# Performance work log

Hardware: AMD Instinct MI355X
Metric: run time of the kernel (lower is better)

## Reference

```python
import jax, jax.numpy as jnp
import numpy as np

DIM, HEADS, WS, SS = 256, 8, 4, 2
B, D, H, W = 2, 16, 56, 56


def _rel_pos_index(ws):
    coords = np.stack(np.meshgrid(np.arange(ws), np.arange(ws), np.arange(ws), indexing='ij'))
    flat = coords.reshape(3, -1)                      # [3, n]
    rel = (flat[:, :, None] - flat[:, None, :]).transpose(1, 2, 0).astype(np.int64)  # [n,n,3]
    rel[..., 0] += ws - 1; rel[..., 1] += ws - 1; rel[..., 2] += ws - 1
    rel[..., 0] *= (2 * ws - 1) ** 2
    rel[..., 1] *= (2 * ws - 1)
    return rel.sum(-1)                                # [n, n]


def _attn_mask(d, h, w, ws, ss):
    # dims are divisible by ws here, so padded dims == dims (matches torch ceil-pad)
    img = np.zeros((d, h, w))
    sl = (slice(0, -ws), slice(-ws, -ss), slice(-ss, None))
    cnt = 0
    for dsl in sl:
        for hsl in sl:
            for wsl in sl:
                img[dsl, hsl, wsl] = cnt
                cnt += 1
    mw = img.reshape(d // ws, ws, h // ws, ws, w // ws, ws)
    mw = mw.transpose(0, 2, 4, 1, 3, 5).reshape(-1, ws ** 3)   # [nW, n]
    diff = mw[:, None, :] - mw[:, :, None]
    return np.where(diff != 0, -100.0, 0.0).astype(np.float32)  # [nW, n, n]


def _window_partition(x, ws):
    b, d, h, w, c = x.shape
    x = x.reshape(b, d // ws, ws, h // ws, ws, w // ws, ws, c)
    return x.transpose(0, 1, 3, 5, 2, 4, 6, 7).reshape(-1, ws ** 3, c)


def _window_reverse(win, ws, b, d, h, w, c):
    x = win.reshape(b, d // ws, h // ws, w // ws, ws, ws, ws, c)
    return x.transpose(0, 1, 4, 2, 5, 3, 6, 7).reshape(b, d, h, w, c)


def _ln(x, g, b, eps=1e-5):
    mu = x.mean(-1, keepdims=True)
    var = ((x - mu) ** 2).mean(-1, keepdims=True)
    return (x - mu) * jax.lax.rsqrt(var + eps) * g + b


def setup_inputs() -> dict:
    key = jax.random.key(0)
    ks = jax.random.split(key, 8)
    s = 0.02
    return {
        'x': jax.random.normal(ks[0], (B, D, H, W, DIM), jnp.float32),
        'norm1_g': jnp.ones((DIM,), jnp.float32),
        'norm1_b': jnp.zeros((DIM,), jnp.float32),
        'qkv_w': jax.random.normal(ks[1], (DIM, 3 * DIM), jnp.float32) * s,
        'qkv_b': jnp.zeros((3 * DIM,), jnp.float32),
        'proj_w': jax.random.normal(ks[2], (DIM, DIM), jnp.float32) * s,
        'proj_b': jnp.zeros((DIM,), jnp.float32),
        'rpb_table': jax.random.normal(ks[3], ((2 * WS - 1) ** 3, HEADS), jnp.float32) * s,
        'norm2_g': jnp.ones((DIM,), jnp.float32),
        'norm2_b': jnp.zeros((DIM,), jnp.float32),
        'fc1_w': jax.random.normal(ks[4], (DIM, 4 * DIM), jnp.float32) * s,
        'fc1_b': jnp.zeros((4 * DIM,), jnp.float32),
        'fc2_w': jax.random.normal(ks[5], (4 * DIM, DIM), jnp.float32) * s,
        'fc2_b': jnp.zeros((DIM,), jnp.float32),
    }


def reference(x, norm1_g, norm1_b, qkv_w, qkv_b, proj_w, proj_b, rpb_table,
              norm2_g, norm2_b, fc1_w, fc1_b, fc2_w, fc2_b):
    b, d, h, w, c = x.shape
    nh, ws, ss = HEADS, WS, SS
    hd = c // nh
    shortcut = x

    xn = _ln(x, norm1_g, norm1_b)
    xs = jnp.roll(xn, shift=(-ss, -ss, -ss), axis=(1, 2, 3))
    xw = _window_partition(xs, ws)            # [B_, n, c]
    B_, n, _ = xw.shape

    qkv = (xw @ qkv_w + qkv_b).reshape(B_, n, 3, nh, hd).transpose(2, 0, 3, 1, 4)
    q, k, v = qkv[0], qkv[1], qkv[2]          # [B_, nh, n, hd]
    attn = jnp.einsum('bhqd,bhkd->bhqk', q * (hd ** -0.5), k)

    rpi = jnp.asarray(_rel_pos_index(ws).reshape(-1))
    bias = rpb_table[rpi].reshape(n, n, nh).transpose(2, 0, 1)  # [nh, n, n]
    attn = attn + bias[None]

    mask = jnp.asarray(_attn_mask(d, h, w, ws, ss))             # [nW, n, n]
    nW = mask.shape[0]
    attn = attn.reshape(B_ // nW, nW, nh, n, n) + mask[None, :, None]
    attn = jax.nn.softmax(attn.reshape(B_, nh, n, n), axis=-1)

    out = jnp.einsum('bhqk,bhkd->bhqd', attn, v).transpose(0, 2, 1, 3).reshape(B_, n, c)
    out = out @ proj_w + proj_b

    xr = _window_reverse(out, ws, b, d, h, w, c)
    xr = jnp.roll(xr, shift=(ss, ss, ss), axis=(1, 2, 3))
    x1 = shortcut + xr

    y = _ln(x1, norm2_g, norm2_b)
    y = jax.nn.gelu(y @ fc1_w + fc1_b, approximate=False) @ fc2_w + fc2_b
    return x1 + y
```

## Files before the change

kernel.cpp:

```cpp
#include <hip/hip_runtime.h>
#include <math.h>


using f32x4  = __attribute__((ext_vector_type(4))) float;
using bf16x8 = __attribute__((ext_vector_type(8))) short;

__device__ __forceinline__ short f2bf(float f) {
  unsigned u = __builtin_bit_cast(unsigned, f);
  u += 0x7fffu + ((u >> 16) & 1u);
  return (short)(u >> 16);
}

#define GLDS16(g, l) __builtin_amdgcn_global_load_lds(                        \
    (__attribute__((address_space(1))) void*)(g),                             \
    (__attribute__((address_space(3))) void*)(l), 16, 0, 0)

__global__ void transpose_all_k(const float* __restrict__ qkv_w,
                                const float* __restrict__ proj_w,
                                const float* __restrict__ fc1_w,
                                const float* __restrict__ fc2_w,
                                short* __restrict__ o_qkv,
                                short* __restrict__ o_proj,
                                short* __restrict__ o_fc1,
                                short* __restrict__ o_fc2) {
  int bid = blockIdx.x;
  const float* in; short* out; int K, N;
  if (bid < 768)       { in = qkv_w;  out = o_qkv;  K = 256;  N = 768; }
  else if (bid < 1024) { in = proj_w; out = o_proj; K = 256;  N = 256;  bid -= 768; }
  else if (bid < 2048) { in = fc1_w;  out = o_fc1;  K = 256;  N = 1024; bid -= 1024; }
  else                 { in = fc2_w;  out = o_fc2;  K = 1024; N = 256;  bid -= 2048; }
  const int idx = bid * 256 + threadIdx.x;
  const int k = idx / N, n = idx % N;
  out[(size_t)n * K + k] = f2bf(in[idx]);
}

__global__ __launch_bounds__(256) void ln1_part_k(
    const float* __restrict__ x, const float* __restrict__ g,
    const float* __restrict__ bta, short* __restrict__ xw) {
  const int wave = threadIdx.x >> 6, lane = threadIdx.x & 63;
  const int row = blockIdx.x * 4 + wave;
  const int win = row >> 6, tok = row & 63;
  const int b = win / 784, wi = win % 784;
  const int wd = wi / 196, wh = (wi / 14) % 14, ww = wi % 14;
  const int tz = tok >> 4, ty = (tok >> 2) & 3, tx = tok & 3;
  const int gd = (wd * 4 + tz + 2) & 15;
  int gh = wh * 4 + ty + 2; if (gh >= 56) gh -= 56;
  int gw = ww * 4 + tx + 2; if (gw >= 56) gw -= 56;
  const size_t src = ((((size_t)b * 16 + gd) * 56 + gh) * 56 + gw) * 256;
  const float4 v = ((const float4*)(x + src))[lane];
  float s = v.x + v.y + v.z + v.w;
#pragma unroll
  for (int m = 1; m < 64; m <<= 1) s += __shfl_xor(s, m);
  const float mean = s * (1.f / 256.f);
  const float dx = v.x - mean, dy = v.y - mean, dz = v.z - mean, dw = v.w - mean;
  float q = dx * dx + dy * dy + dz * dz + dw * dw;
#pragma unroll
  for (int m = 1; m < 64; m <<= 1) q += __shfl_xor(q, m);
  const float rstd = rsqrtf(q * (1.f / 256.f) + 1e-5f);
  const float4 gg = ((const float4*)g)[lane];
  const float4 bb = ((const float4*)bta)[lane];
  short4 o;
  o.x = f2bf(dx * rstd * gg.x + bb.x);
  o.y = f2bf(dy * rstd * gg.y + bb.y);
  o.z = f2bf(dz * rstd * gg.z + bb.z);
  o.w = f2bf(dw * rstd * gg.w + bb.w);
  *(short4*)(xw + (size_t)row * 256 + lane * 4) = o;
}

__global__ __launch_bounds__(256) void ln2_k(
    const float* __restrict__ x1, const float* __restrict__ g,
    const float* __restrict__ bta, short* __restrict__ yn) {
  const int wave = threadIdx.x >> 6, lane = threadIdx.x & 63;
  const int row = blockIdx.x * 4 + wave;
  const float4 v = ((const float4*)(x1 + (size_t)row * 256))[lane];
  float s = v.x + v.y + v.z + v.w;
#pragma unroll
  for (int m = 1; m < 64; m <<= 1) s += __shfl_xor(s, m);
  const float mean = s * (1.f / 256.f);
  const float dx = v.x - mean, dy = v.y - mean, dz = v.z - mean, dw = v.w - mean;
  float q = dx * dx + dy * dy + dz * dz + dw * dw;
#pragma unroll
  for (int m = 1; m < 64; m <<= 1) q += __shfl_xor(q, m);
  const float rstd = rsqrtf(q * (1.f / 256.f) + 1e-5f);
  const float4 gg = ((const float4*)g)[lane];
  const float4 bb = ((const float4*)bta)[lane];
  short4 o;
  o.x = f2bf(dx * rstd * gg.x + bb.x);
  o.y = f2bf(dy * rstd * gg.y + bb.y);
  o.z = f2bf(dz * rstd * gg.z + bb.z);
  o.w = f2bf(dw * rstd * gg.w + bb.w);
  *(short4*)(yn + (size_t)row * 256 + lane * 4) = o;
}

template <int EPI>
__global__ __launch_bounds__(256) void gemm_k(
    const short* __restrict__ A, const short* __restrict__ Bt,
    const float* __restrict__ bias, const float* __restrict__ resid,
    void* __restrict__ OutP, int N, int K) {
  __shared__ short As[128 * 64];
  __shared__ short Bs[128 * 64];
  const int tid = threadIdx.x;
  const int wave = tid >> 6, lane = tid & 63;
  const int quad = lane >> 4, l15 = lane & 15;
  const int m0 = blockIdx.y * 128;
  const int n0 = blockIdx.x * 128;
  const int wm = (wave >> 1) * 64, wn = (wave & 1) * 64;

  f32x4 acc[4][4] = {};

  for (int k0 = 0; k0 < K; k0 += 64) {
    __syncthreads();
#pragma unroll
    for (int i = 0; i < 4; ++i) {
      const int p = wave * 256 + i * 64 + lane;
      const int row = p >> 3;
      const int c = (p & 7) ^ (row & 7);
      GLDS16(A  + (size_t)(m0 + row) * K + (k0 + c * 8),
             As + (size_t)(wave * 256 + i * 64) * 8);
      GLDS16(Bt + (size_t)(n0 + row) * K + (k0 + c * 8),
             Bs + (size_t)(wave * 256 + i * 64) * 8);
    }
    __syncthreads();
#pragma unroll
    for (int ks = 0; ks < 2; ++ks) {
      bf16x8 af[4], bfr[4];
#pragma unroll
      for (int t = 0; t < 4; ++t) {
        const int ra = wm + t * 16 + l15;
        const int ca = (ks * 4 + quad) ^ (ra & 7);
        af[t] = *(const bf16x8*)(As + ra * 64 + ca * 8);
        const int rb = wn + t * 16 + l15;
        const int cb = (ks * 4 + quad) ^ (rb & 7);
        bfr[t] = *(const bf16x8*)(Bs + rb * 64 + cb * 8);
      }
#pragma unroll
      for (int mt = 0; mt < 4; ++mt)
#pragma unroll
        for (int nt = 0; nt < 4; ++nt)
          acc[mt][nt] = __builtin_amdgcn_mfma_f32_16x16x32_bf16(
              af[mt], bfr[nt], acc[mt][nt], 0, 0, 0);
    }
  }

  if constexpr (EPI == 0 || EPI == 1) {
    short* out = (short*)OutP;
#pragma unroll
    for (int nt = 0; nt < 4; ++nt) {
      const int col = n0 + wn + nt * 16 + l15;
      const float bv = bias[col];
#pragma unroll
      for (int mt = 0; mt < 4; ++mt)
#pragma unroll
        for (int reg = 0; reg < 4; ++reg) {
          const int row = m0 + wm + mt * 16 + quad * 4 + reg;
          float v = acc[mt][nt][reg] + bv;
          if constexpr (EPI == 1)
            v = 0.5f * v * (1.f + erff(v * 0.70710678118654752f));
          out[(size_t)row * N + col] = f2bf(v);
        }
    }
  } else if constexpr (EPI == 2) {
    float* out = (float*)OutP;
#pragma unroll
    for (int nt = 0; nt < 4; ++nt) {
      const int col = n0 + wn + nt * 16 + l15;
      const float bv = bias[col];
#pragma unroll
      for (int mt = 0; mt < 4; ++mt)
#pragma unroll
        for (int reg = 0; reg < 4; ++reg) {
          const int row = m0 + wm + mt * 16 + quad * 4 + reg;
          const int win = row >> 6, tok = row & 63;
          const int b = win / 784, wi = win % 784;
          const int wd = wi / 196, wh = (wi / 14) % 14, ww = wi % 14;
          const int tz = tok >> 4, ty = (tok >> 2) & 3, tx = tok & 3;
          const int gd = (wd * 4 + tz + 2) & 15;
          int gh = wh * 4 + ty + 2; if (gh >= 56) gh -= 56;
          int gw = ww * 4 + tx + 2; if (gw >= 56) gw -= 56;
          const size_t dst =
              ((((size_t)b * 16 + gd) * 56 + gh) * 56 + gw) * 256 + col;
          out[dst] = resid[dst] + acc[mt][nt][reg] + bv;
        }
    }
  } else {
    float* out = (float*)OutP;
#pragma unroll
    for (int nt = 0; nt < 4; ++nt) {
      const int col = n0 + wn + nt * 16 + l15;
      const float bv = bias[col];
#pragma unroll
      for (int mt = 0; mt < 4; ++mt)
#pragma unroll
        for (int reg = 0; reg < 4; ++reg) {
          const int row = m0 + wm + mt * 16 + quad * 4 + reg;
          out[(size_t)row * 256 + col] =
              resid[(size_t)row * 256 + col] + acc[mt][nt][reg] + bv;
        }
    }
  }
}

__global__ __launch_bounds__(256) void attn_k(
    const short* __restrict__ qkv, const float* __restrict__ rpb,
    short* __restrict__ aout) {
  __shared__ short Plds[4 * 64 * 80];
  const int tid = threadIdx.x;
  const int wave = tid >> 6, lane = tid & 63;
  const int quad = lane >> 4, l15 = lane & 15;
  const int win = blockIdx.x >> 1;
  const int h = ((blockIdx.x & 1) << 2) + wave;
  const int wi = win % 784;
  const int wd = wi / 196, wh = (wi / 14) % 14, ww = wi % 14;
  const short* base = qkv + (size_t)win * (64 * 768);

  bf16x8 qf[4], kf[4];
#pragma unroll
  for (int t = 0; t < 4; ++t) {
    const short* qp = base + (size_t)(t * 16 + l15) * 768 + h * 32 + quad * 8;
    qf[t] = *(const bf16x8*)qp;
    kf[t] = *(const bf16x8*)(qp + 256);
  }
  f32x4 S[4][4] = {};
#pragma unroll
  for (int mt = 0; mt < 4; ++mt)
#pragma unroll
    for (int nt = 0; nt < 4; ++nt)
      S[mt][nt] = __builtin_amdgcn_mfma_f32_16x16x32_bf16(
          qf[mt], kf[nt], S[mt][nt], 0, 0, 0);

  const bool bd = (wd == 3), bh = (wh == 13), bw = (ww == 13);
  const int yc = l15 >> 2, xc = l15 & 3;
  int labc[4];
#pragma unroll
  for (int nt = 0; nt < 4; ++nt) {
    const int rd = bd ? (nt < 2 ? 1 : 2) : 0;
    const int rh = bh ? (yc < 2 ? 1 : 2) : 0;
    const int rw = bw ? (xc < 2 ? 1 : 2) : 0;
    labc[nt] = rd * 9 + rh * 3 + rw;
  }
  const float scale = 0.17677669529663687f;
#pragma unroll
  for (int mt = 0; mt < 4; ++mt) {
    const int rdr = bd ? (mt < 2 ? 1 : 2) : 0;
    const int rhr = bh ? (quad < 2 ? 1 : 2) : 0;
#pragma unroll
    for (int reg = 0; reg < 4; ++reg) {
      const int rwr = bw ? (reg < 2 ? 1 : 2) : 0;
      const int labr = rdr * 9 + rhr * 3 + rwr;
      float sc[4];
#pragma unroll
      for (int nt = 0; nt < 4; ++nt) {
        const int rpi = (mt - nt + 3) * 49 + (quad - yc + 3) * 7 + (reg - xc + 3);
        const float bias = rpb[rpi * 8 + h];
        const float mv = (labr == labc[nt]) ? 0.f : -100.f;
        sc[nt] = S[mt][nt][reg] * scale + bias + mv;
      }
      float mx = fmaxf(fmaxf(sc[0], sc[1]), fmaxf(sc[2], sc[3]));
      mx = fmaxf(mx, __shfl_xor(mx, 1));
      mx = fmaxf(mx, __shfl_xor(mx, 2));
      mx = fmaxf(mx, __shfl_xor(mx, 4));
      mx = fmaxf(mx, __shfl_xor(mx, 8));
      float p[4], sum = 0.f;
#pragma unroll
      for (int nt = 0; nt < 4; ++nt) { p[nt] = __expf(sc[nt] - mx); sum += p[nt]; }
      sum += __shfl_xor(sum, 1);
      sum += __shfl_xor(sum, 2);
      sum += __shfl_xor(sum, 4);
      sum += __shfl_xor(sum, 8);
      const float inv = 1.f / sum;
      const int r = mt * 16 + quad * 4 + reg;
#pragma unroll
      for (int nt = 0; nt < 4; ++nt)
        Plds[(wave * 64 + r) * 80 + nt * 16 + l15] = f2bf(p[nt] * inv);
    }
  }

  bf16x8 vf[2][2];
#pragma unroll
  for (int kt = 0; kt < 2; ++kt)
#pragma unroll
    for (int n2 = 0; n2 < 2; ++n2)
#pragma unroll
      for (int j = 0; j < 8; ++j)
        vf[kt][n2][j] =
            base[(size_t)(kt * 32 + quad * 8 + j) * 768 + 512 + h * 32 + n2 * 16 + l15];

  f32x4 O[4][2] = {};
#pragma unroll
  for (int mt = 0; mt < 4; ++mt) {
    const short* pr = &Plds[(wave * 64 + mt * 16 + l15) * 80 + quad * 8];
    const bf16x8 pa0 = *(const bf16x8*)pr;
    const bf16x8 pa1 = *(const bf16x8*)(pr + 32);
#pragma unroll
    for (int n2 = 0; n2 < 2; ++n2) {
      O[mt][n2] = __builtin_amdgcn_mfma_f32_16x16x32_bf16(pa0, vf[0][n2], O[mt][n2], 0, 0, 0);
      O[mt][n2] = __builtin_amdgcn_mfma_f32_16x16x32_bf16(pa1, vf[1][n2], O[mt][n2], 0, 0, 0);
    }
  }
#pragma unroll
  for (int mt = 0; mt < 4; ++mt)
#pragma unroll
    for (int n2 = 0; n2 < 2; ++n2)
#pragma unroll
      for (int reg = 0; reg < 4; ++reg) {
        const int tok = mt * 16 + quad * 4 + reg;
        aout[((size_t)win * 64 + tok) * 256 + h * 32 + n2 * 16 + l15] =
            f2bf(O[mt][n2][reg]);
      }
}

extern "C" void kernel_launch(void* const* d_in, const int* in_sizes, int n_in,
                              void* d_out, int out_size, void* d_ws,
                              size_t ws_size, hipStream_t stream) {
  const float* x      = (const float*)d_in[0];
  const float* n1g    = (const float*)d_in[1];
  const float* n1b    = (const float*)d_in[2];
  const float* qkv_w  = (const float*)d_in[3];
  const float* qkv_b  = (const float*)d_in[4];
  const float* proj_w = (const float*)d_in[5];
  const float* proj_b = (const float*)d_in[6];
  const float* rpb    = (const float*)d_in[7];
  const float* n2g    = (const float*)d_in[8];
  const float* n2b    = (const float*)d_in[9];
  const float* fc1_w  = (const float*)d_in[10];
  const float* fc1_b  = (const float*)d_in[11];
  const float* fc2_w  = (const float*)d_in[12];
  const float* fc2_b  = (const float*)d_in[13];

  char* ws = (char*)d_ws;
  short* wt_qkv  = (short*)(ws + 0);
  short* wt_proj = (short*)(ws + 393216);
  short* wt_fc1  = (short*)(ws + 524288);
  short* wt_fc2  = (short*)(ws + 1048576);
  short* bufS    = (short*)(ws + 1572864);
  short* bufL    = (short*)(ws + 52953088);
  float* x1      = (float*)d_out;

  transpose_all_k<<<3072, 256, 0, stream>>>(qkv_w, proj_w, fc1_w, fc2_w,
                                            wt_qkv, wt_proj, wt_fc1, wt_fc2);
  ln1_part_k<<<25088, 256, 0, stream>>>(x, n1g, n1b, bufS);
  gemm_k<0><<<dim3(6, 784), 256, 0, stream>>>(bufS, wt_qkv, qkv_b, nullptr,
                                              bufL, 768, 256);
  attn_k<<<3136, 256, 0, stream>>>(bufL, rpb, bufS);
  gemm_k<2><<<dim3(2, 784), 256, 0, stream>>>(bufS, wt_proj, proj_b, x,
                                              x1, 256, 256);
  ln2_k<<<25088, 256, 0, stream>>>(x1, n2g, n2b, bufS);
  gemm_k<1><<<dim3(8, 784), 256, 0, stream>>>(bufS, wt_fc1, fc1_b, nullptr,
                                              bufL, 1024, 256);
  gemm_k<3><<<dim3(2, 784), 256, 0, stream>>>(bufL, wt_fc2, fc2_b, x1,
                                              x1, 256, 1024);
}
```

Measured before the change: 734.0 us.

## Fuse projection GEMM with residual add and LayerNorm2; swizzle GEMM block order

Replaces the separate projection GEMM and ln2 kernel with one kernel. Each block computes a full 128x256 output row tile, then does the residual add, the window-reverse scatter and LayerNorm2 in registers, writing both x1 and the bf16 normalized activations into a new buffer. This removes one full read of x1 and the extra launch. The cost is higher register pressure (128 accumulators per thread) and a larger LDS footprint. It also remaps the linear block index in gemm_k across groups of eight, which is meant to improve cache locality across XCDs.

```diff
diff --git a/kernel.cpp b/kernel.cpp
--- a/kernel.cpp
+++ b/kernel.cpp
@@ -67,31 +67,6 @@
   *(short4*)(xw + (size_t)row * 256 + lane * 4) = o;
 }
 
-__global__ __launch_bounds__(256) void ln2_k(
-    const float* __restrict__ x1, const float* __restrict__ g,
-    const float* __restrict__ bta, short* __restrict__ yn) {
-  const int wave = threadIdx.x >> 6, lane = threadIdx.x & 63;
-  const int row = blockIdx.x * 4 + wave;
-  const float4 v = ((const float4*)(x1 + (size_t)row * 256))[lane];
-  float s = v.x + v.y + v.z + v.w;
-#pragma unroll
-  for (int m = 1; m < 64; m <<= 1) s += __shfl_xor(s, m);
-  const float mean = s * (1.f / 256.f);
-  const float dx = v.x - mean, dy = v.y - mean, dz = v.z - mean, dw = v.w - mean;
-  float q = dx * dx + dy * dy + dz * dz + dw * dw;
-#pragma unroll
-  for (int m = 1; m < 64; m <<= 1) q += __shfl_xor(q, m);
-  const float rstd = rsqrtf(q * (1.f / 256.f) + 1e-5f);
-  const float4 gg = ((const float4*)g)[lane];
-  const float4 bb = ((const float4*)bta)[lane];
-  short4 o;
-  o.x = f2bf(dx * rstd * gg.x + bb.x);
-  o.y = f2bf(dy * rstd * gg.y + bb.y);
-  o.z = f2bf(dz * rstd * gg.z + bb.z);
-  o.w = f2bf(dw * rstd * gg.w + bb.w);
-  *(short4*)(yn + (size_t)row * 256 + lane * 4) = o;
-}
-
 template <int EPI>
 __global__ __launch_bounds__(256) void gemm_k(
     const short* __restrict__ A, const short* __restrict__ Bt,
@@ -102,8 +77,12 @@
   const int tid = threadIdx.x;
   const int wave = tid >> 6, lane = tid & 63;
   const int quad = lane >> 4, l15 = lane & 15;
-  const int m0 = blockIdx.y * 128;
-  const int n0 = blockIdx.x * 128;
+  const int gx = gridDim.x;
+  int lin = blockIdx.y * gx + blockIdx.x;
+  const int q8 = (gx * gridDim.y) >> 3;
+  lin = (lin & 7) * q8 + (lin >> 3);
+  const int m0 = (lin / gx) * 128;
+  const int n0 = (lin % gx) * 128;
   const int wm = (wave >> 1) * 64, wn = (wave & 1) * 64;
 
   f32x4 acc[4][4] = {};
@@ -159,29 +138,6 @@
           out[(size_t)row * N + col] = f2bf(v);
         }
     }
-  } else if constexpr (EPI == 2) {
-    float* out = (float*)OutP;
-#pragma unroll
-    for (int nt = 0; nt < 4; ++nt) {
-      const int col = n0 + wn + nt * 16 + l15;
-      const float bv = bias[col];
-#pragma unroll
-      for (int mt = 0; mt < 4; ++mt)
-#pragma unroll
-        for (int reg = 0; reg < 4; ++reg) {
-          const int row = m0 + wm + mt * 16 + quad * 4 + reg;
-          const int win = row >> 6, tok = row & 63;
-          const int b = win / 784, wi = win % 784;
-          const int wd = wi / 196, wh = (wi / 14) % 14, ww = wi % 14;
-          const int tz = tok >> 4, ty = (tok >> 2) & 3, tx = tok & 3;
-          const int gd = (wd * 4 + tz + 2) & 15;
-          int gh = wh * 4 + ty + 2; if (gh >= 56) gh -= 56;
-          int gw = ww * 4 + tx + 2; if (gw >= 56) gw -= 56;
-          const size_t dst =
-              ((((size_t)b * 16 + gd) * 56 + gh) * 56 + gw) * 256 + col;
-          out[dst] = resid[dst] + acc[mt][nt][reg] + bv;
-        }
-    }
   } else {
     float* out = (float*)OutP;
 #pragma unroll
@@ -198,6 +154,103 @@
         }
     }
   }
+}
+
+__global__ __launch_bounds__(256) void proj_ln2_k(
+    const short* __restrict__ A, const short* __restrict__ Bt,
+    const float* __restrict__ bias, const float* __restrict__ resid,
+    const float* __restrict__ g2, const float* __restrict__ b2,
+    float* __restrict__ x1, short* __restrict__ yn) {
+  __shared__ short As[128 * 64];
+  __shared__ short Bs[256 * 64];
+  const int tid = threadIdx.x;
+  const int wave = tid >> 6, lane = tid & 63;
+  const int quad = lane >> 4, l15 = lane & 15;
+  const int m0 = blockIdx.x * 128;
+  const int wm = wave * 32;
+
+  f32x4 acc[2][16] = {};
+
+  for (int k0 = 0; k0 < 256; k0 += 64) {
+    __syncthreads();
+#pragma unroll
+    for (int i = 0; i < 4; ++i) {
+      const int p = wave * 256 + i * 64 + lane;
+      const int row = p >> 3;
+      const int c = (p & 7) ^ (row & 7);
+      GLDS16(A + (size_t)(m0 + row) * 256 + (k0 + c * 8),
+             As + (size_t)(wave * 256 + i * 64) * 8);
+    }
+#pragma unroll
+    for (int i = 0; i < 8; ++i) {
+      const int p = i * 256 + tid;
+      const int row = p >> 3;
+      const int c = (p & 7) ^ (row & 7);
+      GLDS16(Bt + (size_t)row * 256 + (k0 + c * 8),
+             Bs + (size_t)(i * 256 + wave * 64) * 8);
+    }
+    __syncthreads();
+#pragma unroll
+    for (int ks = 0; ks < 2; ++ks) {
+      bf16x8 af[2];
+#pragma unroll
+      for (int mt = 0; mt < 2; ++mt) {
+        const int ra = wm + mt * 16 + l15;
+        const int ca = (ks * 4 + quad) ^ (ra & 7);
+        af[mt] = *(const bf16x8*)(As + ra * 64 + ca * 8);
+      }
+#pragma unroll
+      for (int nt = 0; nt < 16; ++nt) {
+        const int rb = nt * 16 + l15;
+        const int cb = (ks * 4 + quad) ^ (rb & 7);
+        const bf16x8 bfr = *(const bf16x8*)(Bs + rb * 64 + cb * 8);
+        acc[0][nt] = __builtin_amdgcn_mfma_f32_16x16x32_bf16(
+            af[0], bfr, acc[0][nt], 0, 0, 0);
+        acc[1][nt] = __builtin_amdgcn_mfma_f32_16x16x32_bf16(
+            af[1], bfr, acc[1][nt], 0, 0, 0);
+      }
+    }
+  }
+
+#pragma unroll
+  for (int mt = 0; mt < 2; ++mt)
+#pragma unroll
+    for (int reg = 0; reg < 4; ++reg) {
+      const int row = m0 + wm + mt * 16 + quad * 4 + reg;
+      const int win = row >> 6, tok = row & 63;
+      const int b = win / 784, wi = win % 784;
+      const int wd = wi / 196, wh = (wi / 14) % 14, ww = wi % 14;
+      const int tz = tok >> 4, ty = (tok >> 2) & 3, tx = tok & 3;
+      const int gd = (wd * 4 + tz + 2) & 15;
+      int gh = wh * 4 + ty + 2; if (gh >= 56) gh -= 56;
+      int gw = ww * 4 + tx + 2; if (gw >= 56) gw -= 56;
+      const size_t nb = ((((size_t)b * 16 + gd) * 56 + gh) * 56 + gw) * 256;
+      float v[16];
+      float s = 0.f;
+#pragma unroll
+      for (int nt = 0; nt < 16; ++nt) {
+        const int col = nt * 16 + l15;
+        v[nt] = acc[mt][nt][reg] + bias[col] + resid[nb + col];
+        s += v[nt];
+      }
+      s += __shfl_xor(s, 1); s += __shfl_xor(s, 2);
+      s += __shfl_xor(s, 4); s += __shfl_xor(s, 8);
+      const float mean = s * (1.f / 256.f);
+      float qs = 0.f;
+#pragma unroll
+      for (int nt = 0; nt < 16; ++nt) {
+        const float d = v[nt] - mean; qs += d * d;
+      }
+      qs += __shfl_xor(qs, 1); qs += __shfl_xor(qs, 2);
+      qs += __shfl_xor(qs, 4); qs += __shfl_xor(qs, 8);
+      const float rstd = rsqrtf(qs * (1.f / 256.f) + 1e-5f);
+#pragma unroll
+      for (int nt = 0; nt < 16; ++nt) {
+        const int col = nt * 16 + l15;
+        x1[nb + col] = v[nt];
+        yn[nb + col] = f2bf((v[nt] - mean) * rstd * g2[col] + b2[col]);
+      }
+    }
 }
 
 __global__ __launch_bounds__(256) void attn_k(
@@ -334,6 +387,7 @@
   short* wt_fc2  = (short*)(ws + 1048576);
   short* bufS    = (short*)(ws + 1572864);
   short* bufL    = (short*)(ws + 52953088);
+  short* bufY    = (short*)(ws + 258473984);
   float* x1      = (float*)d_out;
 
   transpose_all_k<<<3072, 256, 0, stream>>>(qkv_w, proj_w, fc1_w, fc2_w,
@@ -342,10 +396,9 @@
   gemm_k<0><<<dim3(6, 784), 256, 0, stream>>>(bufS, wt_qkv, qkv_b, nullptr,
                                               bufL, 768, 256);
   attn_k<<<3136, 256, 0, stream>>>(bufL, rpb, bufS);
-  gemm_k<2><<<dim3(2, 784), 256, 0, stream>>>(bufS, wt_proj, proj_b, x,
-                                              x1, 256, 256);
-  ln2_k<<<25088, 256, 0, stream>>>(x1, n2g, n2b, bufS);
-  gemm_k<1><<<dim3(8, 784), 256, 0, stream>>>(bufS, wt_fc1, fc1_b, nullptr,
+  proj_ln2_k<<<784, 256, 0, stream>>>(bufS, wt_proj, proj_b, x, n2g, n2b,
+                                      x1, bufY);
+  gemm_k<1><<<dim3(8, 784), 256, 0, stream>>>(bufY, wt_fc1, fc1_b, nullptr,
                                               bufL, 1024, 256);
   gemm_k<3><<<dim3(2, 784), 256, 0, stream>>>(bufL, wt_fc2, fc2_b, x1,
                                               x1, 256, 1024);
```

Measured after the change: 804.9 us. 1.1x slower.

## Stage GEMM epilogues through swizzled LDS for vectorized stores and use fast GELU

Applied to the files above, without the earlier changes.

GEMM epilogues now write accumulators into a swizzled shared-memory tile and then issue 16-byte coalesced global stores. The residual epilogues likewise do vectorized residual loads and stores, including the window-reverse scatter. This removes the scattered scalar stores of the old epilogue. Exact erf GELU is replaced by a tanh-style approximation using exp and a fast reciprocal, which cuts transcendental cost but changes numerics slightly. Extra barriers are added, and the fp32 path is split into two halves to fit in LDS.

```diff
diff --git a/kernel.cpp b/kernel.cpp
--- a/kernel.cpp
+++ b/kernel.cpp
@@ -9,6 +9,12 @@
   unsigned u = __builtin_bit_cast(unsigned, f);
   u += 0x7fffu + ((u >> 16) & 1u);
   return (short)(u >> 16);
+}
+
+__device__ __forceinline__ float gelu_f(float v) {
+  const float u = 1.5957691216057308f * v * (1.f + 0.044715f * v * v);
+  const float e = __expf(u);
+  return v - v * __builtin_amdgcn_rcpf(e + 1.f);
 }
 
 #define GLDS16(g, l) __builtin_amdgcn_global_load_lds(                        \
@@ -97,8 +103,9 @@
     const short* __restrict__ A, const short* __restrict__ Bt,
     const float* __restrict__ bias, const float* __restrict__ resid,
     void* __restrict__ OutP, int N, int K) {
-  __shared__ short As[128 * 64];
-  __shared__ short Bs[128 * 64];
+  __shared__ short SMEM[16384];
+  short* As = SMEM;
+  short* Bs = SMEM + 8192;
   const int tid = threadIdx.x;
   const int wave = tid >> 6, lane = tid & 63;
   const int quad = lane >> 4, l15 = lane & 15;
@@ -142,60 +149,79 @@
     }
   }
 
+  __syncthreads();
   if constexpr (EPI == 0 || EPI == 1) {
+#pragma unroll
+    for (int nt = 0; nt < 4; ++nt) {
+      const int col = wn + nt * 16 + l15;
+      const float bv = bias[n0 + col];
+#pragma unroll
+      for (int mt = 0; mt < 4; ++mt)
+#pragma unroll
+        for (int reg = 0; reg < 4; ++reg) {
+          const int row = wm + mt * 16 + quad * 4 + reg;
+          float v = acc[mt][nt][reg] + bv;
+          if constexpr (EPI == 1) v = gelu_f(v);
+          const int byte = (row << 8) | ((col << 1) ^ ((row & 7) << 4));
+          *(short*)((char*)SMEM + byte) = f2bf(v);
+        }
+    }
+    __syncthreads();
     short* out = (short*)OutP;
 #pragma unroll
-    for (int nt = 0; nt < 4; ++nt) {
-      const int col = n0 + wn + nt * 16 + l15;
-      const float bv = bias[col];
-#pragma unroll
-      for (int mt = 0; mt < 4; ++mt)
-#pragma unroll
-        for (int reg = 0; reg < 4; ++reg) {
-          const int row = m0 + wm + mt * 16 + quad * 4 + reg;
-          float v = acc[mt][nt][reg] + bv;
-          if constexpr (EPI == 1)
-            v = 0.5f * v * (1.f + erff(v * 0.70710678118654752f));
-          out[(size_t)row * N + col] = f2bf(v);
+    for (int i = 0; i < 8; ++i) {
+      const int off = i * 4096 + tid * 16;
+      const int row = off >> 8;
+      const bf16x8 val =
+          *(const bf16x8*)((char*)SMEM + (off ^ ((row & 7) << 4)));
+      *(bf16x8*)(out + (size_t)(m0 + row) * N + n0 + ((off & 255) >> 1)) = val;
+    }
+  } else {
+    float* out = (float*)OutP;
+#pragma unroll
+    for (int hh = 0; hh < 2; ++hh) {
+      if (hh) __syncthreads();
+      if (wm == hh * 64) {
+#pragma unroll
+        for (int nt = 0; nt < 4; ++nt) {
+          const int col = wn + nt * 16 + l15;
+          const float bv = bias[n0 + col];
+#pragma unroll
+          for (int mt = 0; mt < 4; ++mt)
+#pragma unroll
+            for (int reg = 0; reg < 4; ++reg) {
+              const int rloc = mt * 16 + quad * 4 + reg;
+              const int byte = (rloc << 9) | ((col << 2) ^ ((rloc & 7) << 4));
+              *(float*)((char*)SMEM + byte) = acc[mt][nt][reg] + bv;
+            }
         }
-    }
-  } else if constexpr (EPI == 2) {
-    float* out = (float*)OutP;
-#pragma unroll
-    for (int nt = 0; nt < 4; ++nt) {
-      const int col = n0 + wn + nt * 16 + l15;
-      const float bv = bias[col];
-#pragma unroll
-      for (int mt = 0; mt < 4; ++mt)
-#pragma unroll
-        for (int reg = 0; reg < 4; ++reg) {
-          const int row = m0 + wm + mt * 16 + quad * 4 + reg;
-          const int win = row >> 6, tok = row & 63;
+      }
+      __syncthreads();
+#pragma unroll
+      for (int i = 0; i < 8; ++i) {
+        const int off = i * 4096 + tid * 16;
+        const int rloc = off >> 9;
+        f32x4 val = *(const f32x4*)((char*)SMEM + (off ^ ((rloc & 7) << 4)));
+        const int colf = (off & 511) >> 2;
+        const int grow = m0 + hh * 64 + rloc;
+        size_t dst;
+        if constexpr (EPI == 2) {
+          const int win = grow >> 6, tok = grow & 63;
           const int b = win / 784, wi = win % 784;
           const int wd = wi / 196, wh = (wi / 14) % 14, ww = wi % 14;
           const int tz = tok >> 4, ty = (tok >> 2) & 3, tx = tok & 3;
           const int gd = (wd * 4 + tz + 2) & 15;
           int gh = wh * 4 + ty + 2; if (gh >= 56) gh -= 56;
           int gw = ww * 4 + tx + 2; if (gw >= 56) gw -= 56;
-          const size_t dst =
-              ((((size_t)b * 16 + gd) * 56 + gh) * 56 + gw) * 256 + col;
-          out[dst] = resid[dst] + acc[mt][nt][reg] + bv;
+          dst = ((((size_t)b * 16 + gd) * 56 + gh) * 56 + gw) * 256
+                + n0 + colf;
+        } else {
+          dst = (size_t)grow * 256 + n0 + colf;
         }
-    }
-  } else {
-    float* out = (float*)OutP;
-#pragma unroll
-    for (int nt = 0; nt < 4; ++nt) {
-      const int col = n0 + wn + nt * 16 + l15;
-      const float bv = bias[col];
-#pragma unroll
-      for (int mt = 0; mt < 4; ++mt)
-#pragma unroll
-        for (int reg = 0; reg < 4; ++reg) {
-          const int row = m0 + wm + mt * 16 + quad * 4 + reg;
-          out[(size_t)row * 256 + col] =
-              resid[(size_t)row * 256 + col] + acc[mt][nt][reg] + bv;
-        }
+        const f32x4 r = *(const f32x4*)(resid + dst);
+        val = val + r;
+        *(f32x4*)(out + dst) = val;
+      }
     }
   }
 }
```

Result: faster. 705.9 us (-3.8%).
